# Kernel tuning notes

Hardware: AMD Instinct MI355X
Metric: run time of the kernel (lower is better)

Reference implementation:

```python
import jax, jax.numpy as jnp
import numpy as np
import math

D_MODEL = 768
NHEAD = 12
D_HEAD = D_MODEL // NHEAD
TAU = 300.0
NEG = -1e9

def setup_inputs() -> dict:
    key = jax.random.key(0)
    ks = jax.random.split(key, 12)
    N, L, D = 64, 512, D_MODEL
    tokens = jax.random.normal(ks[0], (N, L, D), dtype=jnp.float32)
    ts = jax.random.uniform(ks[1], (N, L, 1), dtype=jnp.float32) * 3600.0  # seconds in a 1h window
    mask = jnp.ones((N, L, 1), dtype=jnp.float32)
    s = 1.0 / math.sqrt(D)
    Wq = jax.random.normal(ks[2], (D, D), dtype=jnp.float32) * s
    bq = jnp.zeros((D,), dtype=jnp.float32)
    Wk = jax.random.normal(ks[3], (D, D), dtype=jnp.float32) * s
    bk = jnp.zeros((D,), dtype=jnp.float32)
    Wv = jax.random.normal(ks[4], (D, D), dtype=jnp.float32) * s
    bv = jnp.zeros((D,), dtype=jnp.float32)
    Wo = jax.random.normal(ks[5], (D, D), dtype=jnp.float32) * s
    bo = jnp.zeros((D,), dtype=jnp.float32)
    readout = jax.random.normal(ks[6], (1, 1, D), dtype=jnp.float32)
    return dict(tokens=tokens, ts=ts, mask=mask, Wq=Wq, bq=bq, Wk=Wk, bk=bk,
                Wv=Wv, bv=bv, Wo=Wo, bo=bo, readout=readout)

def _heads(x, N, L):
    return x.reshape(N, L, NHEAD, D_HEAD).transpose(0, 2, 1, 3)  # (N,H,L,dh)

def reference(tokens, ts, mask, Wq, bq, Wk, bk, Wv, bv, Wo, bo, readout):
    N, L, D = tokens.shape
    scale = 1.0 / math.sqrt(D_HEAD)
    # time-decay bias: log(exp(-|dt|/tau) + 1e-12)
    t = (ts - ts[:, :1, :])[..., 0]                       # (N,L)
    dt = jnp.abs(t[:, :, None] - t[:, None, :])           # (N,L,L)
    bias = jnp.log(jnp.exp(-dt / max(TAU, 1e-6)) + 1e-12)
    q = _heads(tokens @ Wq.T + bq, N, L)
    k = _heads(tokens @ Wk.T + bk, N, L)
    v = _heads(tokens @ Wv.T + bv, N, L)
    attn = jnp.einsum('nhqd,nhkd->nhqk', q, k) * scale + bias[:, None, :, :]
    key_pad = mask[..., 0] <= 0                           # (N,L)
    attn = jnp.where(key_pad[:, None, None, :], NEG, attn)
    A = jax.nn.softmax(attn, axis=-1)
    out = jnp.einsum('nhqk,nhkd->nhqd', A, v).transpose(0, 2, 1, 3).reshape(N, L, D)
    out = (out @ Wo.T + bo) * mask
    # readout pooling attention (single learned query)
    qh = jnp.broadcast_to(readout, (N, 1, D)).reshape(N, 1, NHEAD, D_HEAD).transpose(0, 2, 1, 3)
    kh = _heads(out, N, L)
    pool = jnp.einsum('nhqd,nhkd->nhqk', qh, kh) * scale  # (N,H,1,L)
    pool = jnp.where(key_pad[:, None, None, :], NEG, pool)
    P = jax.nn.softmax(pool, axis=-1)
    pooled = jnp.einsum('nhqk,nhkd->nhqd', P, kh).transpose(0, 2, 1, 3).reshape(N, 1, D)
    return pooled[:, 0, :]
```

## Files before the change

### kernel.cpp

```cpp
#include <hip/hip_runtime.h>
#include <stdint.h>

#define AS1 __attribute__((address_space(1)))
#define AS3 __attribute__((address_space(3)))

typedef __bf16 bf16x8 __attribute__((ext_vector_type(8)));
typedef float  f32x4  __attribute__((ext_vector_type(4)));
typedef float  f32x16 __attribute__((ext_vector_type(16)));

#define MFMA16(a, b, c) __builtin_amdgcn_mfma_f32_16x16x32_bf16((a), (b), (c), 0, 0, 0)
#define MFMA32(a, b, c) __builtin_amdgcn_mfma_f32_32x32x16_bf16((a), (b), (c), 0, 0, 0)

#define SEQ   512
#define NBAT  64
#define DM    768
#define NH    12
#define DH    64
#define NQKV  2304
#define NTOK  (NBAT * SEQ)
#define NKB   12

__device__ __forceinline__ uint16_t f2bf(float x) {
  uint32_t u = __float_as_uint(x);
  return (uint16_t)((u + 0x7FFFu + ((u >> 16) & 1u)) >> 16);
}

__device__ __forceinline__ void async16(uint16_t* lds, const uint16_t* g) {
  __builtin_amdgcn_global_load_lds((AS1 void*)(uintptr_t)(const void*)g,
                                   (AS3 void*)lds, 16, 0, 0);
}

__device__ __forceinline__ int swz(int r) { return (r ^ (r >> 3)) & 7; }

__global__ __launch_bounds__(256) void k_cvt(
    const float* __restrict__ tokens,
    const float* __restrict__ Wq, const float* __restrict__ Wk,
    const float* __restrict__ Wv, const float* __restrict__ Wo,
    const float* __restrict__ bq, const float* __restrict__ bk, const float* __restrict__ bv,
    uint16_t* __restrict__ X, uint16_t* __restrict__ Wqkv_pk, uint16_t* __restrict__ Wob_pk,
    float* __restrict__ bqkv) {
  int i = blockIdx.x * 256 + threadIdx.x;
  {
    const float4* sp = (const float4*)tokens;
    float4 a = sp[2 * i], b = sp[2 * i + 1];
    union { uint16_t u[8]; uint4 v; } o;
    o.u[0] = f2bf(a.x); o.u[1] = f2bf(a.y); o.u[2] = f2bf(a.z); o.u[3] = f2bf(a.w);
    o.u[4] = f2bf(b.x); o.u[5] = f2bf(b.y); o.u[6] = f2bf(b.z); o.u[7] = f2bf(b.w);
    ((uint4*)X)[i] = o.v;
  }
  if (i < 221184) {
    int lane = i & 63, ks = (i >> 6) & 3, kb = (i >> 8) % NKB, g = i / 3072;
    int row = g * 32 + (lane & 31);
    int k   = kb * 64 + ks * 16 + (lane >> 5) * 8;
    const float* src = (row < 768)  ? Wq + (size_t)row * 768 + k
                     : (row < 1536) ? Wk + (size_t)(row - 768) * 768 + k
                                    : Wv + (size_t)(row - 1536) * 768 + k;
    float4 a = *(const float4*)src, b = *(const float4*)(src + 4);
    union { uint16_t u[8]; uint4 v; } o;
    o.u[0] = f2bf(a.x); o.u[1] = f2bf(a.y); o.u[2] = f2bf(a.z); o.u[3] = f2bf(a.w);
    o.u[4] = f2bf(b.x); o.u[5] = f2bf(b.y); o.u[6] = f2bf(b.z); o.u[7] = f2bf(b.w);
    ((uint4*)Wqkv_pk)[i] = o.v;
  }
  if (i < 73728) {
    int lane = i & 63, ks = (i >> 6) & 3, kb = (i >> 8) % NKB, g = i / 3072;
    int row = g * 32 + (lane & 31);
    int k   = kb * 64 + ks * 16 + (lane >> 5) * 8;
    const float* src = Wo + (size_t)row * 768 + k;
    float4 a = *(const float4*)src, b = *(const float4*)(src + 4);
    union { uint16_t u[8]; uint4 v; } o;
    o.u[0] = f2bf(a.x); o.u[1] = f2bf(a.y); o.u[2] = f2bf(a.z); o.u[3] = f2bf(a.w);
    o.u[4] = f2bf(b.x); o.u[5] = f2bf(b.y); o.u[6] = f2bf(b.z); o.u[7] = f2bf(b.w);
    ((uint4*)Wob_pk)[i] = o.v;
  }
  if (i < 768) { bqkv[i] = bq[i]; bqkv[i + 768] = bk[i]; bqkv[i + 1536] = bv[i]; }
}

__global__ __launch_bounds__(256, 4) void k_gemm_bt(
    const uint16_t* __restrict__ A, const uint16_t* __restrict__ Bpk,
    const float* __restrict__ bias, const float* __restrict__ rowscale,
    uint16_t* __restrict__ C, int ldc, int ncol) {
  __shared__ uint16_t Alds[128 * 64];
  const int tid  = threadIdx.x;
  const int w    = tid >> 6, lane = tid & 63;
  const int wu   = __builtin_amdgcn_readfirstlane(w);
  const int l32  = lane & 31, kh = lane >> 5;
  const int sup  = blockIdx.x / (32 * ncol);
  const int t    = blockIdx.x % (32 * ncol);
  const int row0 = (sup * 32 + (t & 31)) * 128, col0 = (t >> 5) * 128;
  const int wrow = (w >> 1) * 64,   wcol = (w & 1) * 64;

  const uint16_t* bw = Bpk + (size_t)((col0 >> 5) + (w & 1) * 2) * (NKB * 2048) + lane * 8;

  f32x16 acc[2][2] = {};
  for (int kb = 0; kb < NKB; ++kb) {
    __syncthreads();
#pragma unroll
    for (int j = 0; j < 4; ++j) {
      int cid = j * 256 + w * 64 + lane;
      int r = cid >> 3, cc = cid & 7, c = cc ^ swz(r);
      async16(&Alds[(j * 256 + wu * 64) * 8],
              A + (size_t)(row0 + r) * 768 + kb * 64 + c * 8);
    }
    __syncthreads();
#pragma unroll
    for (int ks = 0; ks < 4; ++ks) {
      bf16x8 bfr[2];
#pragma unroll
      for (int nt = 0; nt < 2; ++nt)
        bfr[nt] = *(const bf16x8*)(bw + (size_t)nt * (NKB * 2048) + (kb * 4 + ks) * 512);
      bf16x8 af[2];
#pragma unroll
      for (int mt = 0; mt < 2; ++mt) {
        int r = wrow + mt * 32 + l32;
        int c = (ks * 2 + kh) ^ swz(r);
        af[mt] = *(const bf16x8*)&Alds[r * 64 + c * 8];
      }
#pragma unroll
      for (int mt = 0; mt < 2; ++mt)
#pragma unroll
        for (int nt = 0; nt < 2; ++nt)
          acc[mt][nt] = MFMA32(af[mt], bfr[nt], acc[mt][nt]);
    }
  }
#pragma unroll
  for (int nt = 0; nt < 2; ++nt) {
    int col = col0 + wcol + nt * 32 + l32;
    float bv = bias[col];
#pragma unroll
    for (int mt = 0; mt < 2; ++mt) {
#pragma unroll
      for (int rg = 0; rg < 16; ++rg) {
        int row = row0 + wrow + mt * 32 + (rg & 3) + 8 * (rg >> 2) + 4 * kh;
        float v = acc[mt][nt][rg] + bv;
        if (rowscale) v *= rowscale[row];
        C[(size_t)row * ldc + col] = f2bf(v);
      }
    }
  }
}

__global__ __launch_bounds__(256) void k_attn(
    const uint16_t* __restrict__ QKV, const float* __restrict__ ts,
    const float* __restrict__ mask, uint16_t* __restrict__ Aout) {
  __shared__ uint16_t Klds[64 * 64];
  __shared__ uint16_t Vt[64 * 72];
  __shared__ uint16_t Plds[4][2 * 32 * 40];
  __shared__ float tkl[SEQ];

  const int tid = threadIdx.x, w = tid >> 6, lane = tid & 63;
  const int wu = __builtin_amdgcn_readfirstlane(w);
  const int quad = lane >> 4, l16 = lane & 15;
  int b = blockIdx.x;
  int xcd = b & 7, i = b >> 3;
  int qt = i & 3;
  int hg = xcd * 96 + (i >> 2);
  int n = hg / NH, h = hg % NH;
  const int q0 = qt * 128 + w * 32;
  const size_t rowbase = (size_t)n * SEQ * NQKV;

  const float c1 = 0.125f * 1.44269504f;
  const float c2 = 1.44269504f / 300.0f;

  for (int l = tid; l < SEQ; l += 256) {
    float t = ts[n * SEQ + l] * c2;
    tkl[l] = (mask[n * SEQ + l] > 0.f) ? t : 3e38f;
  }

  bf16x8 qf[2][2];
  float tq[2][4];
#pragma unroll
  for (int qs = 0; qs < 2; ++qs) {
    int qr = q0 + qs * 16 + l16;
    const uint16_t* qp = QKV + rowbase + (size_t)qr * NQKV + h * DH;
#pragma unroll
    for (int dsp = 0; dsp < 2; ++dsp)
      qf[qs][dsp] = *(const bf16x8*)(qp + dsp * 32 + quad * 8);
#pragma unroll
    for (int rg = 0; rg < 4; ++rg)
      tq[qs][rg] = ts[n * SEQ + q0 + qs * 16 + quad * 4 + rg] * c2;
  }

  f32x4 accO[2][4] = {};
  f32x4 accL[2] = {};
  bf16x8 ones_b;
  {
    union { uint16_t u[8]; bf16x8 v; } t;
    uint16_t o = (l16 == 0) ? 0x3F80 : 0;
#pragma unroll
    for (int j = 0; j < 8; ++j) t.u[j] = o;
    ones_b = t.v;
  }
  uint16_t* Pw = &Plds[w][0];

  const uint16_t* Kbase = QKV + rowbase + DM + h * DH;
  const uint16_t* Vbase = QKV + rowbase + 2 * DM + h * DH;
  const int vr = tid & 63, vdb = (tid >> 6) * 16;
  uint4 vreg0, vreg1;

#pragma unroll
  for (int j = 0; j < 2; ++j) {
    int cid = j * 256 + w * 64 + lane;
    int r = cid >> 3, cc = cid & 7, c = cc ^ swz(r);
    async16(&Klds[(j * 256 + wu * 64) * 8], Kbase + (size_t)r * NQKV + c * 8);
  }
  vreg0 = *(const uint4*)(Vbase + (size_t)vr * NQKV + vdb);
  vreg1 = *(const uint4*)(Vbase + (size_t)vr * NQKV + vdb + 8);
  __syncthreads();
  {
    union { uint4 v; uint16_t u[8]; } a0, a1;
    a0.v = vreg0; a1.v = vreg1;
#pragma unroll
    for (int j = 0; j < 8; ++j) Vt[(vdb + j) * 72 + vr] = a0.u[j];
#pragma unroll
    for (int j = 0; j < 8; ++j) Vt[(vdb + 8 + j) * 72 + vr] = a1.u[j];
  }
  __syncthreads();

  for (int it = 0; it < 8; ++it) {
    const int k0 = it * 64;
    if (it < 7) {
      vreg0 = *(const uint4*)(Vbase + (size_t)(k0 + 64 + vr) * NQKV + vdb);
      vreg1 = *(const uint4*)(Vbase + (size_t)(k0 + 64 + vr) * NQKV + vdb + 8);
    }

#pragma unroll
    for (int kt = 0; kt < 2; ++kt) {
      uint16_t* Pk = Pw + kt * 1280;
      f32x4 s[2][2] = {};
      __builtin_amdgcn_s_setprio(1);
#pragma unroll
      for (int dsp = 0; dsp < 2; ++dsp) {
        bf16x8 kf[2];
#pragma unroll
        for (int ksu = 0; ksu < 2; ++ksu) {
          int r = kt * 32 + 2 * l16 + ksu;
          int c = (dsp * 4 + quad) ^ swz(r);
          kf[ksu] = *(const bf16x8*)&Klds[r * 64 + c * 8];
        }
#pragma unroll
        for (int qs = 0; qs < 2; ++qs)
#pragma unroll
          for (int ksu = 0; ksu < 2; ++ksu)
            s[qs][ksu] = MFMA16(qf[qs][dsp], kf[ksu], s[qs][ksu]);
      }
      __builtin_amdgcn_s_setprio(0);
      float tk0 = tkl[k0 + kt * 32 + 2 * l16];
      float tk1 = tkl[k0 + kt * 32 + 2 * l16 + 1];
#pragma unroll
      for (int qs = 0; qs < 2; ++qs) {
#pragma unroll
        for (int rg = 0; rg < 4; ++rg) {
          float d0 = fabsf(tq[qs][rg] - tk0);
          float d1 = fabsf(tq[qs][rg] - tk1);
          float p0 = __builtin_amdgcn_exp2f(fmaf(s[qs][0][rg], c1, -d0));
          float p1 = __builtin_amdgcn_exp2f(fmaf(s[qs][1][rg], c1, -d1));
          uint32_t u = (__float_as_uint(p0) >> 16) | (__float_as_uint(p1) & 0xFFFF0000u);
          *(uint32_t*)(Pk + (qs * 16 + quad * 4 + rg) * 40 + 2 * l16) = u;
        }
      }
      asm volatile("" ::: "memory");
      __builtin_amdgcn_sched_barrier(0);
      bf16x8 vb[4];
#pragma unroll
      for (int dt = 0; dt < 4; ++dt)
        vb[dt] = *(const bf16x8*)&Vt[(dt * 16 + l16) * 72 + kt * 32 + quad * 8];
      __builtin_amdgcn_s_setprio(1);
#pragma unroll
      for (int qs = 0; qs < 2; ++qs) {
        bf16x8 pa = *(const bf16x8*)(Pk + (qs * 16 + l16) * 40 + quad * 8);
#pragma unroll
        for (int dt = 0; dt < 4; ++dt)
          accO[qs][dt] = MFMA16(pa, vb[dt], accO[qs][dt]);
        accL[qs] = MFMA16(pa, ones_b, accL[qs]);
      }
      __builtin_amdgcn_s_setprio(0);
      asm volatile("" ::: "memory");
      __builtin_amdgcn_sched_barrier(0);
    }

    __syncthreads();
    if (it < 7) {
      {
        union { uint4 v; uint16_t u[8]; } a0, a1;
        a0.v = vreg0; a1.v = vreg1;
#pragma unroll
        for (int j = 0; j < 8; ++j) Vt[(vdb + j) * 72 + vr] = a0.u[j];
#pragma unroll
        for (int j = 0; j < 8; ++j) Vt[(vdb + 8 + j) * 72 + vr] = a1.u[j];
      }
#pragma unroll
      for (int j = 0; j < 2; ++j) {
        int cid = j * 256 + w * 64 + lane;
        int r = cid >> 3, cc = cid & 7, c = cc ^ swz(r);
        async16(&Klds[(j * 256 + wu * 64) * 8],
                Kbase + (size_t)(k0 + 64 + r) * NQKV + c * 8);
      }
    }
    __syncthreads();
  }
#pragma unroll
  for (int qs = 0; qs < 2; ++qs) {
    float inv[4];
#pragma unroll
    for (int rg = 0; rg < 4; ++rg) {
      float lv = __shfl(accL[qs][rg], lane & 48, 64);
      inv[rg] = 1.0f / lv;
    }
#pragma unroll
    for (int dt = 0; dt < 4; ++dt) {
#pragma unroll
      for (int rg = 0; rg < 4; ++rg) {
        int qr = q0 + qs * 16 + quad * 4 + rg;
        float v = accO[qs][dt][rg] * inv[rg];
        Aout[(size_t)(n * SEQ + qr) * DM + h * DH + dt * 16 + l16] = f2bf(v);
      }
    }
  }
}

__global__ __launch_bounds__(256) void k_pool(
    const uint16_t* __restrict__ Out, const float* __restrict__ mask,
    const float* __restrict__ readout, float* __restrict__ dst) {
  __shared__ float rsl[64];
  __shared__ float ex[SEQ];
  __shared__ float red[4];
  __shared__ float part[8][64];
  int b = blockIdx.x;
  int n = b / NH, h = b % NH;
  int tid = threadIdx.x;
  if (tid < 64) rsl[tid] = readout[h * DH + tid];
  __syncthreads();

  float suml = 0.f;
  for (int l = tid; l < SEQ; l += 256) {
    const uint16_t* rowp = Out + (size_t)(n * SEQ + l) * DM + h * DH;
    float acc = 0.f;
#pragma unroll
    for (int c = 0; c < 8; ++c) {
      union { uint4 v; uint16_t u[8]; } t;
      t.v = *(const uint4*)(rowp + c * 8);
#pragma unroll
      for (int j = 0; j < 8; ++j)
        acc += __uint_as_float(((uint32_t)t.u[j]) << 16) * rsl[c * 8 + j];
    }
    float e = __builtin_amdgcn_exp2f(acc * (0.125f * 1.44269504f));
    e = (mask[n * SEQ + l] > 0.f) ? e : 0.f;
    ex[l] = e;
    suml += e;
  }
#pragma unroll
  for (int off = 32; off; off >>= 1) suml += __shfl_down(suml, off, 64);
  if ((tid & 63) == 0) red[tid >> 6] = suml;
  __syncthreads();
  float inv = 1.0f / (red[0] + red[1] + red[2] + red[3]);

  int d0 = (tid & 31) * 2, ch = tid >> 5;
  float a0 = 0.f, a1 = 0.f;
  for (int l = ch * 64; l < ch * 64 + 64; ++l) {
    uint32_t pv = *(const uint32_t*)(Out + (size_t)(n * SEQ + l) * DM + h * DH + d0);
    float e = ex[l];
    a0 = fmaf(__uint_as_float(pv << 16), e, a0);
    a1 = fmaf(__uint_as_float(pv & 0xFFFF0000u), e, a1);
  }
  part[ch][d0] = a0;
  part[ch][d0 + 1] = a1;
  __syncthreads();
  if (tid < 64) {
    float s = 0.f;
#pragma unroll
    for (int c = 0; c < 8; ++c) s += part[c][tid];
    dst[n * DM + h * DH + tid] = s * inv;
  }
}

extern "C" void kernel_launch(void* const* d_in, const int* in_sizes, int n_in,
                              void* d_out, int out_size, void* d_ws, size_t ws_size,
                              hipStream_t stream) {
  const float* tokens  = (const float*)d_in[0];
  const float* ts      = (const float*)d_in[1];
  const float* mask    = (const float*)d_in[2];
  const float* Wq      = (const float*)d_in[3];
  const float* bq      = (const float*)d_in[4];
  const float* Wk      = (const float*)d_in[5];
  const float* bk      = (const float*)d_in[6];
  const float* Wv      = (const float*)d_in[7];
  const float* bv      = (const float*)d_in[8];
  const float* Wo      = (const float*)d_in[9];
  const float* bo      = (const float*)d_in[10];
  const float* readout = (const float*)d_in[11];

  char* ws = (char*)d_ws;
  uint16_t* X    = (uint16_t*)ws;
  uint16_t* Wqkv = (uint16_t*)(ws + 50331648);
  uint16_t* Wob  = (uint16_t*)(ws + 53870592);
  float*    bqkv = (float*)   (ws + 55050240);
  uint16_t* QKV  = (uint16_t*)(ws + 55059456);
  uint16_t* attn = X;
  uint16_t* Outb = QKV;

  k_cvt<<<12288, 256, 0, stream>>>(tokens, Wq, Wk, Wv, Wo, bq, bk, bv, X, Wqkv, Wob, bqkv);
  k_gemm_bt<<<4608, 256, 0, stream>>>(X, Wqkv, bqkv, nullptr, QKV, NQKV, 18);
  k_attn<<<3072, 256, 0, stream>>>(QKV, ts, mask, attn);
  k_gemm_bt<<<1536, 256, 0, stream>>>(attn, Wob, bo, mask, Outb, DM, 6);
  k_pool<<<768, 256, 0, stream>>>(Outb, mask, readout, (float*)d_out);
}
```

Measured before the change: 481.6 us.

## Double attention block to 512 threads covering 256 queries per K/V tile

The attention kernel now launches 8 waves per block instead of 4, so each block handles two 128-query tiles of the same (batch, head) and shares every K/V tile loaded into LDS across twice as many queries. The grid is halved and each thread loads half as much K/V per iteration. This cuts redundant global K/V traffic and staging work per query. In exchange, LDS per block grows (Plds doubles), which may reduce resident blocks per CU, and more waves wait at each barrier.

Measured after the change: 478.4 us. About the same (-0.7%).

```diff
diff --git a/kernel.cpp b/kernel.cpp
--- a/kernel.cpp
+++ b/kernel.cpp
@@ -139,12 +139,12 @@
   }
 }
 
-__global__ __launch_bounds__(256) void k_attn(
+__global__ __launch_bounds__(512) void k_attn(
     const uint16_t* __restrict__ QKV, const float* __restrict__ ts,
     const float* __restrict__ mask, uint16_t* __restrict__ Aout) {
   __shared__ uint16_t Klds[64 * 64];
   __shared__ uint16_t Vt[64 * 72];
-  __shared__ uint16_t Plds[4][2 * 32 * 40];
+  __shared__ uint16_t Plds[8][2 * 32 * 40];
   __shared__ float tkl[SEQ];
 
   const int tid = threadIdx.x, w = tid >> 6, lane = tid & 63;
@@ -152,16 +152,16 @@
   const int quad = lane >> 4, l16 = lane & 15;
   int b = blockIdx.x;
   int xcd = b & 7, i = b >> 3;
-  int qt = i & 3;
-  int hg = xcd * 96 + (i >> 2);
+  int qtp = i & 1;
+  int hg = xcd * 96 + (i >> 1);
   int n = hg / NH, h = hg % NH;
-  const int q0 = qt * 128 + w * 32;
+  const int q0 = (qtp * 2 + (w >> 2)) * 128 + (w & 3) * 32;
   const size_t rowbase = (size_t)n * SEQ * NQKV;
 
   const float c1 = 0.125f * 1.44269504f;
   const float c2 = 1.44269504f / 300.0f;
 
-  for (int l = tid; l < SEQ; l += 256) {
+  for (int l = tid; l < SEQ; l += 512) {
     float t = ts[n * SEQ + l] * c2;
     tkl[l] = (mask[n * SEQ + l] > 0.f) ? t : 3e38f;
   }
@@ -194,34 +194,27 @@
 
   const uint16_t* Kbase = QKV + rowbase + DM + h * DH;
   const uint16_t* Vbase = QKV + rowbase + 2 * DM + h * DH;
-  const int vr = tid & 63, vdb = (tid >> 6) * 16;
-  uint4 vreg0, vreg1;
-
-#pragma unroll
-  for (int j = 0; j < 2; ++j) {
-    int cid = j * 256 + w * 64 + lane;
-    int r = cid >> 3, cc = cid & 7, c = cc ^ swz(r);
-    async16(&Klds[(j * 256 + wu * 64) * 8], Kbase + (size_t)r * NQKV + c * 8);
+  const int vr = tid & 63, vdb = (tid >> 6) * 8;
+  uint4 vreg0;
+
+  {
+    int r = tid >> 3, c = (tid & 7) ^ swz(tid >> 3);
+    async16(&Klds[wu * 64 * 8], Kbase + (size_t)r * NQKV + c * 8);
   }
   vreg0 = *(const uint4*)(Vbase + (size_t)vr * NQKV + vdb);
-  vreg1 = *(const uint4*)(Vbase + (size_t)vr * NQKV + vdb + 8);
   __syncthreads();
   {
-    union { uint4 v; uint16_t u[8]; } a0, a1;
-    a0.v = vreg0; a1.v = vreg1;
+    union { uint4 v; uint16_t u[8]; } a0;
+    a0.v = vreg0;
 #pragma unroll
     for (int j = 0; j < 8; ++j) Vt[(vdb + j) * 72 + vr] = a0.u[j];
-#pragma unroll
-    for (int j = 0; j < 8; ++j) Vt[(vdb + 8 + j) * 72 + vr] = a1.u[j];
   }
   __syncthreads();
 
   for (int it = 0; it < 8; ++it) {
     const int k0 = it * 64;
-    if (it < 7) {
+    if (it < 7)
       vreg0 = *(const uint4*)(Vbase + (size_t)(k0 + 64 + vr) * NQKV + vdb);
-      vreg1 = *(const uint4*)(Vbase + (size_t)(k0 + 64 + vr) * NQKV + vdb + 8);
-    }
 
 #pragma unroll
     for (int kt = 0; kt < 2; ++kt) {
@@ -281,19 +274,14 @@
     __syncthreads();
     if (it < 7) {
       {
-        union { uint4 v; uint16_t u[8]; } a0, a1;
-        a0.v = vreg0; a1.v = vreg1;
+        union { uint4 v; uint16_t u[8]; } a0;
+        a0.v = vreg0;
 #pragma unroll
         for (int j = 0; j < 8; ++j) Vt[(vdb + j) * 72 + vr] = a0.u[j];
-#pragma unroll
-        for (int j = 0; j < 8; ++j) Vt[(vdb + 8 + j) * 72 + vr] = a1.u[j];
-      }
-#pragma unroll
-      for (int j = 0; j < 2; ++j) {
-        int cid = j * 256 + w * 64 + lane;
-        int r = cid >> 3, cc = cid & 7, c = cc ^ swz(r);
-        async16(&Klds[(j * 256 + wu * 64) * 8],
-                Kbase + (size_t)(k0 + 64 + r) * NQKV + c * 8);
+      }
+      {
+        int r = tid >> 3, c = (tid & 7) ^ swz(tid >> 3);
+        async16(&Klds[wu * 64 * 8], Kbase + (size_t)(k0 + 64 + r) * NQKV + c * 8);
       }
     }
     __syncthreads();
@@ -400,7 +388,7 @@
 
   k_cvt<<<12288, 256, 0, stream>>>(tokens, Wq, Wk, Wv, Wo, bq, bk, bv, X, Wqkv, Wob, bqkv);
   k_gemm_bt<<<4608, 256, 0, stream>>>(X, Wqkv, bqkv, nullptr, QKV, NQKV, 18);
-  k_attn<<<3072, 256, 0, stream>>>(QKV, ts, mask, attn);
+  k_attn<<<1536, 512, 0, stream>>>(QKV, ts, mask, attn);
   k_gemm_bt<<<1536, 256, 0, stream>>>(attn, Wob, bo, mask, Outb, DM, 6);
   k_pool<<<768, 256, 0, stream>>>(Outb, mask, readout, (float*)d_out);
 }
```
